# Optimization experiments

Hardware: AMD Instinct MI355X
Metric: run time of the kernel (lower is better)

Reference implementation:

```python
import jax, jax.numpy as jnp
import numpy as np

N, E, EL = 20000, 320000, 100000
IN, HID, OUT, H = 256, 128, 128, 4
NEG_SLOPE = 0.2


def setup_inputs() -> dict:
    key = jax.random.key(0)
    ks = jax.random.split(key, 20)
    g = lambda k, shape, fan: jax.random.normal(k, shape, jnp.float32) * (1.0 / np.sqrt(fan))
    inp = {
        'x': jax.random.normal(ks[0], (N, IN), jnp.float32),
        'edge_index': jax.random.randint(ks[1], (2, E), 0, N, jnp.int32),
        'edge_label_index': jax.random.randint(ks[2], (2, EL), 0, N, jnp.int32),
        # GATv2 layer 1: in -> hidden, heads=H, concat
        'W_l1': g(ks[3], (IN, H * HID), IN), 'b_l1': jnp.zeros((H * HID,), jnp.float32),
        'W_r1': g(ks[4], (IN, H * HID), IN), 'b_r1': jnp.zeros((H * HID,), jnp.float32),
        'att1': g(ks[5], (H, HID), HID), 'bias1': jnp.zeros((H * HID,), jnp.float32),
        # GATv2 layer 2: H*hidden -> out, heads=1
        'W_l2': g(ks[6], (H * HID, OUT), H * HID), 'b_l2': jnp.zeros((OUT,), jnp.float32),
        'W_r2': g(ks[7], (H * HID, OUT), H * HID), 'b_r2': jnp.zeros((OUT,), jnp.float32),
        'att2': g(ks[8], (1, OUT), OUT), 'bias2': jnp.zeros((OUT,), jnp.float32),
        # decoder: Linear(2*OUT, HID) -> GELU -> Linear(HID, 1)
        'W_d1': g(ks[9], (2 * OUT, HID), 2 * OUT), 'b_d1': jnp.zeros((HID,), jnp.float32),
        'W_d2': g(ks[10], (HID, 1), HID), 'b_d2': jnp.zeros((1,), jnp.float32),
    }
    return inp


def gatv2_conv(x, src, dst, Wl, bl, Wr, br, att, bias, heads, ch):
    n = x.shape[0]
    xl = (x @ Wl + bl).reshape(n, heads, ch)  # source transform
    xr = (x @ Wr + br).reshape(n, heads, ch)  # target transform
    xj = xl[src]                              # [E, H, C] messages from source
    xi = xr[dst]                              # [E, H, C]
    e = jax.nn.leaky_relu(xi + xj, NEG_SLOPE)
    logits = jnp.einsum('ehc,hc->eh', e, att)  # [E, H]
    # segment softmax over incoming edges of each target node
    m = jax.ops.segment_max(logits, dst, num_segments=n)
    a = jnp.exp(logits - m[dst])
    s = jax.ops.segment_sum(a, dst, num_segments=n)
    alpha = a / s[dst]
    out = jax.ops.segment_sum(alpha[..., None] * xj, dst, num_segments=n)
    return out.reshape(n, heads * ch) + bias


def reference(x, edge_index, edge_label_index,
              W_l1, b_l1, W_r1, b_r1, att1, bias1,
              W_l2, b_l2, W_r2, b_r2, att2, bias2,
              W_d1, b_d1, W_d2, b_d2):
    n = x.shape[0]
    loops = jnp.arange(n, dtype=edge_index.dtype)
    src = jnp.concatenate([edge_index[0], loops])  # add_self_loops=True (PyG default)
    dst = jnp.concatenate([edge_index[1], loops])
    z = gatv2_conv(x, src, dst, W_l1, b_l1, W_r1, b_r1, att1, bias1, H, HID)
    z = jax.nn.gelu(z)  # dropout is identity in eval mode
    z = gatv2_conv(z, src, dst, W_l2, b_l2, W_r2, b_r2, att2, bias2, 1, OUT)
    # link decoder: gather-concat-MLP
    h = jnp.concatenate([z[edge_label_index[0]], z[edge_label_index[1]]], axis=-1)
    h = jax.nn.gelu(h @ W_d1 + b_d1)
    return (h @ W_d2 + b_d2).squeeze(-1)
```

## Files before the change

kernel.cpp:

```cpp
#include <hip/hip_runtime.h>
#include <hip/hip_bf16.h>
#include <math.h>
#include <stdint.h>

using bf16 = __hip_bfloat16;
typedef unsigned short u16;
typedef unsigned int   u32;
typedef __attribute__((ext_vector_type(8))) short short8;
typedef __attribute__((ext_vector_type(4))) float f32x4;

static constexpr int NN   = 20000;
static constexpr int EE   = 320000;
static constexpr int ELN  = 100000;
static constexpr int ETOT = EE + NN;
static constexpr int INC  = 256;
static constexpr int C1   = 512;
static constexpr int C2   = 128;
static constexpr int NB   = (NN + 255) / 256;

__device__ __forceinline__ float us2f(u16 u){ union{u32 i; float f;}x; x.i=((u32)u)<<16; return x.f; }
__device__ __forceinline__ u16  f2us(float f){ union{bf16 h; u16 u;}c; c.h=__float2bfloat16(f); return c.u; }
__device__ __forceinline__ float h2f(u16 u){ union{u16 u; _Float16 h;}c; c.u=u; return (float)c.h; }
__device__ __forceinline__ float gelu_f(float x){
  float u = 1.5957691216057308f*(x + 0.044715f*x*x*x);
  float ex = __expf(u);
  float th = 1.f - 2.f/(ex + 1.f);
  return 0.5f*x*(1.f+th);
}
__device__ __forceinline__ void ld4v(const float* p, float* o){ float4 v=*(const float4*)p; o[0]=v.x;o[1]=v.y;o[2]=v.z;o[3]=v.w; }
__device__ __forceinline__ void ld4v(const u16* p, float* o){ uint2 v=*(const uint2*)p;
  o[0]=us2f(v.x&0xffff);o[1]=us2f(v.x>>16);o[2]=us2f(v.y&0xffff);o[3]=us2f(v.y>>16); }
__device__ __forceinline__ void ld4v(const _Float16* p, float* o){ uint2 v=*(const uint2*)p;
  o[0]=h2f(v.x&0xffff);o[1]=h2f(v.x>>16);o[2]=h2f(v.y&0xffff);o[3]=h2f(v.y>>16); }
__device__ __forceinline__ void ld8v(const float* p, float* o){ ld4v(p,o); ld4v(p+4,o+4); }
__device__ __forceinline__ void ld8v(const u16* p, float* o){ uint4 v=*(const uint4*)p;
  o[0]=us2f(v.x&0xffff);o[1]=us2f(v.x>>16);o[2]=us2f(v.y&0xffff);o[3]=us2f(v.y>>16);
  o[4]=us2f(v.z&0xffff);o[5]=us2f(v.z>>16);o[6]=us2f(v.w&0xffff);o[7]=us2f(v.w>>16); }
__device__ __forceinline__ void ld8v(const _Float16* p, float* o){ uint4 v=*(const uint4*)p;
  o[0]=h2f(v.x&0xffff);o[1]=h2f(v.x>>16);o[2]=h2f(v.y&0xffff);o[3]=h2f(v.y>>16);
  o[4]=h2f(v.z&0xffff);o[5]=h2f(v.z>>16);o[6]=h2f(v.w&0xffff);o[7]=h2f(v.w>>16); }
__device__ __forceinline__ void ld2v(const float* p, float* o){ float2 v=*(const float2*)p; o[0]=v.x;o[1]=v.y; }
__device__ __forceinline__ void ld2v(const _Float16* p, float* o){ u32 w=*(const u32*)p;
  o[0]=h2f(w&0xffff); o[1]=h2f(w>>16); }
__device__ __forceinline__ void st4v(float* p, const float* v){ *(float4*)p = make_float4(v[0],v[1],v[2],v[3]); }
__device__ __forceinline__ void st4v(u16* p, const float* v){ uint2 o;
  o.x=f2us(v[0])|((u32)f2us(v[1])<<16); o.y=f2us(v[2])|((u32)f2us(v[3])<<16); *(uint2*)p=o; }
__device__ __forceinline__ void st8v(float* p, const float* v){ st4v(p,v); st4v(p+4,v+4); }
__device__ __forceinline__ void st8v(u16* p, const float* v){ uint4 o;
  o.x=f2us(v[0])|((u32)f2us(v[1])<<16); o.y=f2us(v[2])|((u32)f2us(v[3])<<16);
  o.z=f2us(v[4])|((u32)f2us(v[5])<<16); o.w=f2us(v[6])|((u32)f2us(v[7])<<16); *(uint4*)p=o; }
__device__ __forceinline__ void st8v(_Float16* p, const float* v){
  union{ _Float16 h[8]; uint4 u; } c;
  #pragma unroll
  for (int j=0;j<8;++j) c.h[j] = (_Float16)v[j];
  *(uint4*)p = c.u; }

__global__ void k_hist(const int* __restrict__ ei, int* __restrict__ cnt) {
  int e = blockIdx.x*blockDim.x + threadIdx.x;
  if (e < ETOT) {
    int d = (e < EE) ? ei[EE + e] : (e - EE);
    if ((u32)d < (u32)NN) atomicAdd(&cnt[d], 1);
  }
}
__global__ void k_scan_a(const int* __restrict__ cnt, int* __restrict__ row_ptr,
                         int* __restrict__ bsum) {
  __shared__ int buf[256];
  int idx = blockIdx.x*256 + threadIdx.x;
  int v = (idx < NN) ? cnt[idx] : 0;
  buf[threadIdx.x] = v;
  __syncthreads();
  for (int off = 1; off < 256; off <<= 1) {
    int t = (threadIdx.x >= off) ? buf[threadIdx.x - off] : 0;
    __syncthreads();
    buf[threadIdx.x] += t;
    __syncthreads();
  }
  if (idx < NN) row_ptr[idx] = buf[threadIdx.x] - v;
  if (threadIdx.x == 255) bsum[blockIdx.x] = buf[255];
// ... 38 lines not shown
                                                int n) {
  for (int i = blockIdx.x*256 + threadIdx.x; i < n; i += gridDim.x*256) {
    float v = A[i];
    u16 h = f2us(v);
    Ath[i] = h;
    Atl[i] = f2us(v - us2f(h));
  }
}

struct WsArgs { const float* src[5]; u16* th[5]; u16* tl[5]; int K[5]; int N[5]; };
__global__ __launch_bounds__(256) void k_wsplit_all(WsArgs a) {
  int seg = blockIdx.y;
  int K = a.K[seg], N = a.N[seg];
  int n = K * N;
  int idx = blockIdx.x*256 + threadIdx.x;
  if (idx >= n) return;
  int nn = idx / K, k = idx - nn*K;
  float v = a.src[seg][(size_t)k*N + nn];
  u16 h = f2us(v);
  a.th[seg][idx] = h;
  a.tl[seg][idx] = f2us(v - us2f(h));
}

template <typename CT>
__global__ __launch_bounds__(256, 2)
void k_mgemm_p(const u16* __restrict__ Ath, const u16* __restrict__ Atl,
               const u16* __restrict__ Bth, const u16* __restrict__ Btl,
               const float* __restrict__ biasA, const float* __restrict__ biasB, int ncut,
               CT* __restrict__ C, int M, int N, int K) {
  __shared__ __align__(16) u16 Ah[128][32], Al[128][32];
  __shared__ __align__(16) u16 Bh[128][32], Bl[128][32];
  int tid = threadIdx.x;
  int m0 = blockIdx.x * 128, n0 = blockIdx.y * 128;
  int wave = tid >> 6, lane = tid & 63;
  int wm = (wave & 1) * 64, wn = (wave >> 1) * 64;
  int l15 = lane & 15, quad = lane >> 4;
  f32x4 acc[4][4] = {};
  int ar = tid >> 1;
  int ac = (tid & 1) * 16;
  int bn = tid >> 2;
  int bc = (tid & 3) * 8;
  uint4 z4 = make_uint4(0,0,0,0);
  for (int k0 = 0; k0 < K; k0 += 32) {
    int gr = m0 + ar;
    if (gr < M) {
      const u16* ph = &Ath[(size_t)gr*K + k0 + ac];
      const u16* pl = &Atl[(size_t)gr*K + k0 + ac];
      *(uint4*)&Ah[ar][ac]   = *(const uint4*)ph;
      *(uint4*)&Ah[ar][ac+8] = *(const uint4*)(ph+8);
      *(uint4*)&Al[ar][ac]   = *(const uint4*)pl;
      *(uint4*)&Al[ar][ac+8] = *(const uint4*)(pl+8);
    } else {
      *(uint4*)&Ah[ar][ac] = z4; *(uint4*)&Ah[ar][ac+8] = z4;
      *(uint4*)&Al[ar][ac] = z4; *(uint4*)&Al[ar][ac+8] = z4;
    }
    #pragma unroll
    for (int i = 0; i < 2; ++i) {
      int n = bn + 64*i;
      *(uint4*)&Bh[n][bc] = *(const uint4*)&Bth[(size_t)(n0+n)*K + k0 + bc];
      *(uint4*)&Bl[n][bc] = *(const uint4*)&Btl[(size_t)(n0+n)*K + k0 + bc];
    }
    __syncthreads();
    short8 af_h[4], af_l[4], bf_h[4], bf_l[4];
    #pragma unroll
    for (int i = 0; i < 4; ++i) {
      af_h[i] = *(const short8*)&Ah[wm + i*16 + l15][quad*8];
      af_l[i] = *(const short8*)&Al[wm + i*16 + l15][quad*8];
      bf_h[i] = *(const short8*)&Bh[wn + i*16 + l15][quad*8];
      bf_l[i] = *(const short8*)&Bl[wn + i*16 + l15][quad*8];
    }
    #pragma unroll
    for (int i = 0; i < 4; ++i)
      #pragma unroll
      for (int j = 0; j < 4; ++j) {
        acc[i][j] = __builtin_amdgcn_mfma_f32_16x16x32_bf16(af_h[i], bf_l[j], acc[i][j], 0,0,0);
        acc[i][j] = __builtin_amdgcn_mfma_f32_16x16x32_bf16(af_l[i], bf_h[j], acc[i][j], 0,0,0);
        acc[i][j] = __builtin_amdgcn_mfma_f32_16x16x32_bf16(af_h[i], bf_h[j], acc[i][j], 0,0,0);
      }
    __syncthreads();
  }
  #pragma unroll
  for (int j = 0; j < 4; ++j) {
    int col = n0 + wn + j*16 + l15;
    float bv = (col < ncut) ? biasA[col] : biasB[col - ncut];
    #pragma unroll
    for (int i = 0; i < 4; ++i) {
      int rbase = m0 + wm + i*16 + quad*4;
      #pragma unroll
      for (int r = 0; r < 4; ++r) {
        int row = rbase + r;
        if (row < M) C[(size_t)row*N + col] = (CT)(acc[i][j][r] + bv);
      }
    }
  }
}

template <typename AT, typename CT>
__global__ __launch_bounds__(256, 2)
void k_mgemm(const AT* __restrict__ A,
             const u16* __restrict__ Bth, const u16* __restrict__ Btl,
             const float* __restrict__ biasA, const float* __restrict__ biasB, int ncut,
             CT* __restrict__ C, int M, int N, int K) {
  __shared__ __align__(16) u16 Ah[128][32], Al[128][32];
  __shared__ __align__(16) u16 Bh[128][32], Bl[128][32];
  int tid = threadIdx.x;
  int m0 = blockIdx.x * 128, n0 = blockIdx.y * 128;
  int wave = tid >> 6, lane = tid & 63;
  int wm = (wave & 1) * 64, wn = (wave >> 1) * 64;
  int l15 = lane & 15, quad = lane >> 4;
  f32x4 acc[4][4] = {};
  int ar = tid >> 3;
  int ak = (tid & 7) * 4;
  int bn = tid >> 2;
  int bc = (tid & 3) * 8;
  for (int k0 = 0; k0 < K; k0 += 32) {
    #pragma unroll
    for (int i = 0; i < 4; ++i) {
      int row = ar + 32*i;
      int gr = m0 + row;
      float hv[4] = {0.f, 0.f, 0.f, 0.f};
      if (gr < M) ld4v(&A[(size_t)gr*K + k0 + ak], hv);
      u16 hi[4], lo[4];
      #pragma unroll
      for (int j = 0; j < 4; ++j) {
        hi[j] = f2us(hv[j]);
        lo[j] = f2us(hv[j] - us2f(hi[j]));
      }
      *(uint2*)&Ah[row][ak] = make_uint2(hi[0]|((u32)hi[1]<<16), hi[2]|((u32)hi[3]<<16));
      *(uint2*)&Al[row][ak] = make_uint2(lo[0]|((u32)lo[1]<<16), lo[2]|((u32)lo[3]<<16));
    }
    #pragma unroll
    for (int i = 0; i < 2; ++i) {
      int n = bn + 64*i;
      *(uint4*)&Bh[n][bc] = *(const uint4*)&Bth[(size_t)(n0+n)*K + k0 + bc];
      *(uint4*)&Bl[n][bc] = *(const uint4*)&Btl[(size_t)(n0+n)*K + k0 + bc];
    }
    __syncthreads();
    short8 af_h[4], af_l[4], bf_h[4], bf_l[4];
    #pragma unroll
    for (int i = 0; i < 4; ++i) {
      af_h[i] = *(const short8*)&Ah[wm + i*16 + l15][quad*8];
      af_l[i] = *(const short8*)&Al[wm + i*16 + l15][quad*8];
      bf_h[i] = *(const short8*)&Bh[wn + i*16 + l15][quad*8];
      bf_l[i] = *(const short8*)&Bl[wn + i*16 + l15][quad*8];
    }
    #pragma unroll
    for (int i = 0; i < 4; ++i)
      #pragma unroll
      for (int j = 0; j < 4; ++j) {
        acc[i][j] = __builtin_amdgcn_mfma_f32_16x16x32_bf16(af_h[i], bf_l[j], acc[i][j], 0,0,0);
        acc[i][j] = __builtin_amdgcn_mfma_f32_16x16x32_bf16(af_l[i], bf_h[j], acc[i][j], 0,0,0);
        acc[i][j] = __builtin_amdgcn_mfma_f32_16x16x32_bf16(af_h[i], bf_h[j], acc[i][j], 0,0,0);
      }
    __syncthreads();
  }
  #pragma unroll
  for (int j = 0; j < 4; ++j) {
    int col = n0 + wn + j*16 + l15;
    float bv = (col < ncut) ? biasA[col] : biasB[col - ncut];
    #pragma unroll
    for (int i = 0; i < 4; ++i) {
      int rbase = m0 + wm + i*16 + quad*4;
      #pragma unroll
      for (int r = 0; r < 4; ++r) {
        int row = rbase + r;
        if (row < M) C[(size_t)row*N + col] = (CT)(acc[i][j][r] + bv);
      }
    }
  }
}

__global__ __launch_bounds__(256, 2)
void k_dec3(const _Float16* __restrict__ z2,
            const int* __restrict__ eli,
            const u16* __restrict__ Wth, const u16* __restrict__ Wtl,
            const float* __restrict__ bd1,
            const float* __restrict__ Wd2, const float* __restrict__ bd2,
            float* __restrict__ out) {
  __shared__ __align__(16) u16 Ah[128][32], Al[128][32];
  __shared__ __align__(16) u16 Bh[128][32], Bl[128][32];
  __shared__ float pr[128][2];
  int tid = threadIdx.x;
  int e0 = blockIdx.x * 128;
  int wave = tid >> 6, lane = tid & 63;
  int wm = (wave & 1) * 64, wn = (wave >> 1) * 64;
  int l15 = lane & 15, quad = lane >> 4;
  int ar = tid >> 3;
  int ak = (tid & 7) * 4;
  int bn = tid >> 2;
  int bc = (tid & 3) * 8;
  int ia4[4], ib4[4];
  #pragma unroll
  for (int i = 0; i < 4; ++i) {
    int e = e0 + ar + 32*i;
    bool ev = e < ELN;
    int a = ev ? eli[e] : 0;      if ((u32)a >= (u32)NN) a = 0;
    int b = ev ? eli[ELN+e] : 0;  if ((u32)b >= (u32)NN) b = 0;
    ia4[i] = a; ib4[i] = b;
  }
  f32x4 acc[4][4] = {};
  for (int k0 = 0; k0 < 256; k0 += 32) {
    #pragma unroll
    for (int i = 0; i < 4; ++i) {
      int row = ar + 32*i;
      int kk = k0 + ak;
      const _Float16* src = (kk < 128) ? &z2[(size_t)ia4[i]*128 + kk]
                                       : &z2[(size_t)ib4[i]*128 + (kk - 128)];
      float hv[4];
      ld4v(src, hv);
      u16 hi[4], lo[4];
      #pragma unroll
      for (int j = 0; j < 4; ++j) {
        hi[j] = f2us(hv[j]);
        lo[j] = f2us(hv[j] - us2f(hi[j]));
      }
      *(uint2*)&Ah[row][ak] = make_uint2(hi[0]|((u32)hi[1]<<16), hi[2]|((u32)hi[3]<<16));
      *(uint2*)&Al[row][ak] = make_uint2(lo[0]|((u32)lo[1]<<16), lo[2]|((u32)lo[3]<<16));
    }
    #pragma unroll
    for (int i = 0; i < 2; ++i) {
      int n = bn + 64*i;
      *(uint4*)&Bh[n][bc] = *(const uint4*)&Wth[(size_t)n*256 + k0 + bc];
      *(uint4*)&Bl[n][bc] = *(const uint4*)&Wtl[(size_t)n*256 + k0 + bc];
    }
    __syncthreads();
    short8 af_h[4], af_l[4], bf_h[4], bf_l[4];
    #pragma unroll
    for (int i = 0; i < 4; ++i) {
      af_h[i] = *(const short8*)&Ah[wm + i*16 + l15][quad*8];
      af_l[i] = *(const short8*)&Al[wm + i*16 + l15][quad*8];
      bf_h[i] = *(const short8*)&Bh[wn + i*16 + l15][quad*8];
      bf_l[i] = *(const short8*)&Bl[wn + i*16 + l15][quad*8];
    }
    #pragma unroll
    for (int i = 0; i < 4; ++i)
      #pragma unroll
      for (int j = 0; j < 4; ++j) {
        acc[i][j] = __builtin_amdgcn_mfma_f32_16x16x32_bf16(af_h[i], bf_l[j], acc[i][j], 0,0,0);
        acc[i][j] = __builtin_amdgcn_mfma_f32_16x16x32_bf16(af_l[i], bf_h[j], acc[i][j], 0,0,0);
        acc[i][j] = __builtin_amdgcn_mfma_f32_16x16x32_bf16(af_h[i], bf_h[j], acc[i][j], 0,0,0);
      }
    __syncthreads();
  }
  float w2c[4], bbc[4];
  #pragma unroll
  for (int j = 0; j < 4; ++j) {
    int col = wn + j*16 + l15;
    w2c[j] = Wd2[col];
    bbc[j] = bd1[col];
  }
  #pragma unroll
  for (int i = 0; i < 4; ++i) {
    #pragma unroll
    for (int r = 0; r < 4; ++r) {
      float part = 0.f;
      #pragma unroll
      for (int j = 0; j < 4; ++j)
        part += gelu_f(acc[i][j][r] + bbc[j]) * w2c[j];
      part += __shfl_xor(part,1); part += __shfl_xor(part,2);
      part += __shfl_xor(part,4); part += __shfl_xor(part,8);
      if (l15 == 0) pr[wm + i*16 + quad*4 + r][wn>>6] = part;
    }
  }
  __syncthreads();
  if (tid < 128) {
    int e = e0 + tid;
    if (e < ELN) out[e] = pr[tid][0] + pr[tid][1] + bd2[0];
  }
}

template <typename AT, typename CT>
__global__ __launch_bounds__(256) void k_gemm(const AT* __restrict__ A,
                                              const float* __restrict__ W,
                                              const float* __restrict__ bias,
                                              CT* __restrict__ C,
                                              int M, int Nc, int K) {
  __shared__ __align__(16) float As[16][64];
  __shared__ __align__(16) float Bs[16][64];
  int tid = threadIdx.x;
  int m0 = blockIdx.x*64, n0 = blockIdx.y*64;
  int ty = tid >> 4, tx = tid & 15;
  int lrow = tid >> 2;
  int lk   = (tid & 3)*4;
  int wk   = tid >> 4;
  int wn   = (tid & 15)*4;
  float acc[4][4] = {};
  for (int k0 = 0; k0 < K; k0 += 16) {
    int row = m0 + lrow;
    if (row < M) {
      float a4[4]; ld4v(&A[(size_t)row*K + k0 + lk], a4);
      As[lk+0][lrow]=a4[0]; As[lk+1][lrow]=a4[1]; As[lk+2][lrow]=a4[2]; As[lk+3][lrow]=a4[3];
    } else {
      #pragma unroll
      for (int j=0;j<4;++j) As[lk+j][lrow]=0.f;
    }
    {
      float4 bv4 = *(const float4*)&W[(size_t)(k0+wk)*Nc + n0 + wn];
      Bs[wk][wn+0]=bv4.x; Bs[wk][wn+1]=bv4.y; Bs[wk][wn+2]=bv4.z; Bs[wk][wn+3]=bv4.w;
    }
    __syncthreads();
    #pragma unroll
    for (int kk=0;kk<16;++kk) {
      float4 av = *(const float4*)&As[kk][ty*4];
      float4 bv = *(const float4*)&Bs[kk][tx*4];
      float a[4]={av.x,av.y,av.z,av.w}, b[4]={bv.x,bv.y,bv.z,bv.w};
      #pragma unroll
      for (int i=0;i<4;++i)
        #pragma unroll
        for (int j=0;j<4;++j)
          acc[i][j] += a[i]*b[j];
    }
    __syncthreads();
  }
  float bv[4];
  #pragma unroll
  for (int j=0;j<4;++j) bv[j] = bias[n0 + tx*4 + j];
  #pragma unroll
  for (int i=0;i<4;++i) {
    int row = m0 + ty*4 + i;
    if (row < M) {
      float o4[4] = {acc[i][0]+bv[0], acc[i][1]+bv[1], acc[i][2]+bv[2], acc[i][3]+bv[3]};
      st4v(&C[(size_t)row*Nc + n0 + tx*4], o4);
    }
  }
}

template <typename TI, typename TO>
__global__ __launch_bounds__(256) void k_edge1(const TI* __restrict__ xl,
                                               const TI* __restrict__ xr, int ld,
                                               const float* __restrict__ att,
                                               const float* __restrict__ bias,
                                               const int* __restrict__ row_ptr,
                                               const int* __restrict__ col,
                                               TO* __restrict__ z1) {
  int wid = (blockIdx.x*blockDim.x + threadIdx.x) >> 6;
  if (wid >= NN) return;
  int lane = threadIdx.x & 63;
  int c8 = lane*8;
  float xi[8], av[8], acc[8] = {};
  ld8v(&xr[(size_t)wid*ld + c8], xi);
  #pragma unroll
  for (int j=0;j<8;++j) av[j] = att[c8+j];
  float s = 0.f;
  int e0 = row_ptr[wid], e1 = row_ptr[wid+1];
  int e = e0;
  if ((e1 - e0) & 1) {
    int sn = col[e]; if ((u32)sn >= (u32)NN) sn = 0;
    float xj[8];
    ld8v(&xl[(size_t)sn*ld + c8], xj);
    float p = 0.f;
    #pragma unroll
    for (int j=0;j<8;++j) {
      float t = xi[j] + xj[j];
      t = fmaxf(t, 0.2f*t);
      p += t*av[j];
    }
    p += __shfl_xor(p,1); p += __shfl_xor(p,2);
// ... 6 lines not shown
  }
  for (; e < e1; e += 2) {
    int s1 = col[e];   if ((u32)s1 >= (u32)NN) s1 = 0;
    int s2 = col[e+1]; if ((u32)s2 >= (u32)NN) s2 = 0;
    float xj1[8], xj2[8];
    ld8v(&xl[(size_t)s1*ld + c8], xj1);
    ld8v(&xl[(size_t)s2*ld + c8], xj2);
    float p1 = 0.f, p2 = 0.f;
    #pragma unroll
    for (int j=0;j<8;++j) {
      float t1 = xi[j] + xj1[j]; t1 = fmaxf(t1, 0.2f*t1); p1 += t1*av[j];
      float t2 = xi[j] + xj2[j]; t2 = fmaxf(t2, 0.2f*t2); p2 += t2*av[j];
    }
    p1 += __shfl_xor(p1,1); p2 += __shfl_xor(p2,1);
    p1 += __shfl_xor(p1,2); p2 += __shfl_xor(p2,2);
    p1 += __shfl_xor(p1,4); p2 += __shfl_xor(p2,4);
    p1 += __shfl_xor(p1,8); p2 += __shfl_xor(p2,8);
    float w1 = __expf(p1);
    float w2 = __expf(p2);
    s += w1 + w2;
    #pragma unroll
    for (int j=0;j<8;++j) acc[j] += w1*xj1[j] + w2*xj2[j];
  }
  float inv = 1.f/s, o[8];
  #pragma unroll
  for (int j=0;j<8;++j) o[j] = gelu_f(acc[j]*inv + bias[c8+j]);
  st8v(&z1[(size_t)wid*C1 + c8], o);
}

template <typename TI, typename TO>
__global__ __launch_bounds__(256) void k_edge2(const TI* __restrict__ xl,
                                               const TI* __restrict__ xr, int ld,
                                               const float* __restrict__ att,
                                               const float* __restrict__ bias,
                                               const int* __restrict__ row_ptr,
                                               const int* __restrict__ col,
                                               TO* __restrict__ z2) {
  int wid = (blockIdx.x*blockDim.x + threadIdx.x) >> 6;
  if (wid >= NN) return;
  int lane = threadIdx.x & 63;
  int c2 = lane*2;
  float xiv[2];
  ld2v(&xr[(size_t)wid*ld + c2], xiv);
  float a0 = att[c2], a1 = att[c2+1];
  float s = 0.f, ac0 = 0.f, ac1 = 0.f;
  int e0 = row_ptr[wid], e1 = row_ptr[wid+1];
  int e = e0;
  if ((e1 - e0) & 1) {
    int sn = col[e]; if ((u32)sn >= (u32)NN) sn = 0;
    float xj[2];
    ld2v(&xl[(size_t)sn*ld + c2], xj);
    float t0 = xiv[0] + xj[0]; t0 = fmaxf(t0, 0.2f*t0);
    float t1 = xiv[1] + xj[1]; t1 = fmaxf(t1, 0.2f*t1);
    float p = t0*a0 + t1*a1;
    p += __shfl_xor(p,1);  p += __shfl_xor(p,2);
    p += __shfl_xor(p,4);  p += __shfl_xor(p,8);
    p += __shfl_xor(p,16); p += __shfl_xor(p,32);
    float w = __expf(p);
    s += w;
    ac0 += w*xj[0];
// ... 3 lines not shown
  for (; e < e1; e += 2) {
    int s1 = col[e];   if ((u32)s1 >= (u32)NN) s1 = 0;
    int s2 = col[e+1]; if ((u32)s2 >= (u32)NN) s2 = 0;
    float xj1[2], xj2[2];
    ld2v(&xl[(size_t)s1*ld + c2], xj1);
    ld2v(&xl[(size_t)s2*ld + c2], xj2);
    float u0 = xiv[0] + xj1[0]; u0 = fmaxf(u0, 0.2f*u0);
    float u1 = xiv[1] + xj1[1]; u1 = fmaxf(u1, 0.2f*u1);
    float v0 = xiv[0] + xj2[0]; v0 = fmaxf(v0, 0.2f*v0);
    float v1 = xiv[1] + xj2[1]; v1 = fmaxf(v1, 0.2f*v1);
    float p1 = u0*a0 + u1*a1;
    float p2 = v0*a0 + v1*a1;
    p1 += __shfl_xor(p1,1);  p2 += __shfl_xor(p2,1);
    p1 += __shfl_xor(p1,2);  p2 += __shfl_xor(p2,2);
    p1 += __shfl_xor(p1,4);  p2 += __shfl_xor(p2,4);
    p1 += __shfl_xor(p1,8);  p2 += __shfl_xor(p2,8);
    p1 += __shfl_xor(p1,16); p2 += __shfl_xor(p2,16);
    p1 += __shfl_xor(p1,32); p2 += __shfl_xor(p2,32);
    float w1 = __expf(p1);
    float w2 = __expf(p2);
    s += w1 + w2;
    ac0 += w1*xj1[0] + w2*xj2[0];
    ac1 += w1*xj1[1] + w2*xj2[1];
  }
  float inv = 1.f/s;
  z2[(size_t)wid*C2 + c2]   = (TO)(ac0*inv + bias[c2]);
  z2[(size_t)wid*C2 + c2+1] = (TO)(ac1*inv + bias[c2+1]);
}

__global__ __launch_bounds__(256) void k_dec2(const float* __restrict__ z2,
                                              const int* __restrict__ eli,
                                              const float* __restrict__ Wd1,
                                              const float* __restrict__ bd1,
                                              const float* __restrict__ Wd2,
                                              const float* __restrict__ bd2,
                                              float* __restrict__ out) {
  __shared__ __align__(16) float As[16][64];
  __shared__ __align__(16) float Bs[16][128];
  int tid = threadIdx.x;
  int e0 = blockIdx.x * 64;
  int ty = tid >> 4, tx = tid & 15;
  int lrow = tid >> 2;
  int lk   = (tid & 3) * 4;
  int wk   = tid >> 4;
  int wn   = (tid & 15) * 8;
  int e = e0 + lrow;
// ... 84 lines not shown
    k_tiny<<<1, 64, 0, stream>>>(out, 16384.f + (float)mb);
    return;
  }

  size_t regA = full ? (size_t)NN*C1 : (size_t)NN*C1/2;
  char* base = (char*)d_ws;
  void* wA = base;
  void* wB = base + regA*4;
  void* wC = base + 2*regA*4;
  int* row_ptr = (int*)(base + 3*regA*4);
  int* cnt     = row_ptr + (NN + 1);
  int* col     = cnt + NN;
  int* bsum    = (int*)wA;

  hipMemsetAsync(cnt, 0, NN*sizeof(int), stream);
  k_hist<<<(ETOT+255)/256, 256, 0, stream>>>(ei, cnt);
  k_scan_a<<<NB, 256, 0, stream>>>(cnt, row_ptr, bsum);
  k_scan_b<<<1, 128, 0, stream>>>(bsum, row_ptr);
  k_scan_c<<<NB, 256, 0, stream>>>(row_ptr, bsum, cnt);
  k_scatter<<<(ETOT+255)/256, 256, 0, stream>>>(ei, cnt, col);

  if (full) {
    _Float16* xlr1 = (_Float16*)wA;
    _Float16* z1   = (_Float16*)wC;
    _Float16* xlr2 = (_Float16*)wA;
    _Float16* z2   = (_Float16*)wC;
    u16* xth = (u16*)wB;
    u16* xtl = xth + (size_t)NN*INC;
    u16* wt1th = (u16*)((char*)wB + (21u<<20));
    u16* wt1tl = wt1th + 1024*256;
    u16* wt2th = wt1tl + 1024*256;
    u16* wt2tl = wt2th + 256*512;
    u16* wdth  = wt2tl + 256*512;
    u16* wdtl  = wdth  + 128*256;

    k_xsplit<<<2048, 256, 0, stream>>>(x, xth, xtl, NN*INC);
    WsArgs wa;
    wa.src[0]=Wl1; wa.th[0]=wt1th;          wa.tl[0]=wt1tl;          wa.K[0]=INC; wa.N[0]=C1;
    wa.src[1]=Wr1; wa.th[1]=wt1th+512*256;  wa.tl[1]=wt1tl+512*256;  wa.K[1]=INC; wa.N[1]=C1;
    wa.src[2]=Wl2; wa.th[2]=wt2th;          wa.tl[2]=wt2tl;          wa.K[2]=C1;  wa.N[2]=C2;
    wa.src[3]=Wr2; wa.th[3]=wt2th+128*512;  wa.tl[3]=wt2tl+128*512;  wa.K[3]=C1;  wa.N[3]=C2;
    wa.src[4]=Wd1; wa.th[4]=wdth;           wa.tl[4]=wdtl;           wa.K[4]=256; wa.N[4]=C2;
    k_wsplit_all<<<dim3(512, 5), 256, 0, stream>>>(wa);

    dim3 gm1((NN+127)/128, 1024/128);
    k_mgemm_p<_Float16><<<gm1, 256, 0, stream>>>(xth, xtl, wt1th, wt1tl,
                                                 bl1, br1, 512, xlr1, NN, 1024, INC);
    k_edge1<_Float16,_Float16><<<NN/4, 256, 0, stream>>>(xlr1, xlr1+512, 1024,
                                                         att1, bias1, row_ptr, col, z1);
    dim3 gm2((NN+127)/128, 256/128);
    k_mgemm<_Float16,_Float16><<<gm2, 256, 0, stream>>>(z1, wt2th, wt2tl,
                                                        bl2, br2, 128, xlr2, NN, 256, C1);
    k_edge2<_Float16,_Float16><<<NN/4, 256, 0, stream>>>(xlr2, xlr2+128, 256,
                                                         att2, bias2, row_ptr, col, z2);
    k_dec3<<<(ELN+127)/128, 256, 0, stream>>>(z2, eli, wdth, wdtl, bd1, Wd2, bd2, out);
  } else {
    u16* xl1 = (u16*)wA;
    u16* xr1 = (u16*)wB;
    u16* z1  = (u16*)wC;
    float* xl2 = (float*)wA;
    float* xr2 = (float*)wB;
    float* z2  = (float*)wC;
    dim3 g1((NN+63)/64, C1/64);
    dim3 g2((NN+63)/64, C2/64);
    k_gemm<float,u16><<<g1, 256, 0, stream>>>(x, Wl1, bl1, xl1, NN, C1, INC);
    k_gemm<float,u16><<<g1, 256, 0, stream>>>(x, Wr1, br1, xr1, NN, C1, INC);
    k_edge1<u16,u16><<<NN/4, 256, 0, stream>>>(xl1, xr1, C1, att1, bias1, row_ptr, col, z1);
    k_gemm<u16,float><<<g2, 256, 0, stream>>>(z1, Wl2, bl2, xl2, NN, C2, C1);
    k_gemm<u16,float><<<g2, 256, 0, stream>>>(z1, Wr2, br2, xr2, NN, C2, C1);
    k_edge2<float,float><<<NN/4, 256, 0, stream>>>(xl2, xr2, C2, att2, bias2, row_ptr, col, z2);
    k_dec2<<<(ELN+63)/64, 256, 0, stream>>>(z2, eli, Wd1, bd1, Wd2, bd2, out);
  }
}
```

Baseline: 392.2 us.

## Load GEMM tiles directly to LDS and emit pre-split bf16 activations from edge kernels

The MFMA GEMMs now stage A/B tiles with global_load_lds (direct global-to-LDS copies), one wave per operand, instead of register round-trips. The edge kernels write outputs pre-split into bf16 hi/lo pairs, so the layer-2 GEMM and decoder no longer split activations on the fly. The GEMM epilogue goes through LDS for coalesced 128-bit stores, and block indexing is remapped so N-tiles of the same M-rows run adjacently. The costs are double the bytes for the z1/z2 intermediates and a serial load-sync-compute loop with no double buffering.

Result: no change. 389.0 us (-0.8%).

```diff
diff --git a/kernel.cpp b/kernel.cpp
--- a/kernel.cpp
+++ b/kernel.cpp
@@ -27,11 +27,13 @@
   float th = 1.f - 2.f/(ex + 1.f);
   return 0.5f*x*(1.f+th);
 }
+__device__ __forceinline__ void gl_lds16(const u16* g, void* l) {
+  __builtin_amdgcn_global_load_lds((const __attribute__((address_space(1))) void*)g,
+                                   (__attribute__((address_space(3))) void*)l, 16, 0, 0);
+}
 __device__ __forceinline__ void ld4v(const float* p, float* o){ float4 v=*(const float4*)p; o[0]=v.x;o[1]=v.y;o[2]=v.z;o[3]=v.w; }
 __device__ __forceinline__ void ld4v(const u16* p, float* o){ uint2 v=*(const uint2*)p;
   o[0]=us2f(v.x&0xffff);o[1]=us2f(v.x>>16);o[2]=us2f(v.y&0xffff);o[3]=us2f(v.y>>16); }
-__device__ __forceinline__ void ld4v(const _Float16* p, float* o){ uint2 v=*(const uint2*)p;
-  o[0]=h2f(v.x&0xffff);o[1]=h2f(v.x>>16);o[2]=h2f(v.y&0xffff);o[3]=h2f(v.y>>16); }
 __device__ __forceinline__ void ld8v(const float* p, float* o){ ld4v(p,o); ld4v(p+4,o+4); }
 __device__ __forceinline__ void ld8v(const u16* p, float* o){ uint4 v=*(const uint4*)p;
   o[0]=us2f(v.x&0xffff);o[1]=us2f(v.x>>16);o[2]=us2f(v.y&0xffff);o[3]=us2f(v.y>>16);
@@ -49,11 +51,6 @@
 __device__ __forceinline__ void st8v(u16* p, const float* v){ uint4 o;
   o.x=f2us(v[0])|((u32)f2us(v[1])<<16); o.y=f2us(v[2])|((u32)f2us(v[3])<<16);
   o.z=f2us(v[4])|((u32)f2us(v[5])<<16); o.w=f2us(v[6])|((u32)f2us(v[7])<<16); *(uint4*)p=o; }
-__device__ __forceinline__ void st8v(_Float16* p, const float* v){
-  union{ _Float16 h[8]; uint4 u; } c;
-  #pragma unroll
-  for (int j=0;j<8;++j) c.h[j] = (_Float16)v[j];
-  *(uint4*)p = c.u; }
 
 __global__ void k_hist(const int* __restrict__ ei, int* __restrict__ cnt) {
   int e = blockIdx.x*blockDim.x + threadIdx.x;
@@ -138,52 +135,39 @@
   a.tl[seg][idx] = f2us(v - us2f(h));
 }
 
-template <typename CT>
 __global__ __launch_bounds__(256, 2)
-void k_mgemm_p(const u16* __restrict__ Ath, const u16* __restrict__ Atl,
+void k_mgemm_a(const u16* __restrict__ Ath, const u16* __restrict__ Atl,
                const u16* __restrict__ Bth, const u16* __restrict__ Btl,
                const float* __restrict__ biasA, const float* __restrict__ biasB, int ncut,
-               CT* __restrict__ C, int M, int N, int K) {
-  __shared__ __align__(16) u16 Ah[128][32], Al[128][32];
-  __shared__ __align__(16) u16 Bh[128][32], Bl[128][32];
+               _Float16* __restrict__ C, int M, int N, int K, int nby) {
+  __shared__ __align__(16) u16 sm[17408];
   int tid = threadIdx.x;
-  int m0 = blockIdx.x * 128, n0 = blockIdx.y * 128;
+  int bidy = blockIdx.x % nby, bidx = blockIdx.x / nby;
+  int m0 = bidx * 128, n0 = bidy * 128;
   int wave = tid >> 6, lane = tid & 63;
   int wm = (wave & 1) * 64, wn = (wave >> 1) * 64;
   int l15 = lane & 15, quad = lane >> 4;
+  const u16* pbase = (wave == 0) ? Ath : (wave == 1) ? Atl : (wave == 2) ? Bth : Btl;
+  bool isA = wave < 2;
+  int rbase = isA ? m0 : n0;
+  int rseg = lane >> 2;
+  int kseg = (lane & 3) * 8;
   f32x4 acc[4][4] = {};
-  int ar = tid >> 1;
-  int ac = (tid & 1) * 16;
-  int bn = tid >> 2;
-  int bc = (tid & 3) * 8;
-  uint4 z4 = make_uint4(0,0,0,0);
   for (int k0 = 0; k0 < K; k0 += 32) {
-    int gr = m0 + ar;
-    if (gr < M) {
-      const u16* ph = &Ath[(size_t)gr*K + k0 + ac];
-      const u16* pl = &Atl[(size_t)gr*K + k0 + ac];
-      *(uint4*)&Ah[ar][ac]   = *(const uint4*)ph;
-      *(uint4*)&Ah[ar][ac+8] = *(const uint4*)(ph+8);
-      *(uint4*)&Al[ar][ac]   = *(const uint4*)pl;
-      *(uint4*)&Al[ar][ac+8] = *(const uint4*)(pl+8);
-    } else {
-      *(uint4*)&Ah[ar][ac] = z4; *(uint4*)&Ah[ar][ac+8] = z4;
-      *(uint4*)&Al[ar][ac] = z4; *(uint4*)&Al[ar][ac+8] = z4;
-    }
-    #pragma unroll
-    for (int i = 0; i < 2; ++i) {
-      int n = bn + 64*i;
-      *(uint4*)&Bh[n][bc] = *(const uint4*)&Bth[(size_t)(n0+n)*K + k0 + bc];
-      *(uint4*)&Bl[n][bc] = *(const uint4*)&Btl[(size_t)(n0+n)*K + k0 + bc];
+    #pragma unroll
+    for (int i = 0; i < 8; ++i) {
+      int r = rbase + i*16 + rseg;
+      if (isA && r > M-1) r = M-1;
+      gl_lds16(&pbase[(size_t)r*K + k0 + kseg], (char*)sm + (wave<<13) + (i<<10));
     }
     __syncthreads();
     short8 af_h[4], af_l[4], bf_h[4], bf_l[4];
     #pragma unroll
     for (int i = 0; i < 4; ++i) {
-      af_h[i] = *(const short8*)&Ah[wm + i*16 + l15][quad*8];
-      af_l[i] = *(const short8*)&Al[wm + i*16 + l15][quad*8];
-      bf_h[i] = *(const short8*)&Bh[wn + i*16 + l15][quad*8];
-      bf_l[i] = *(const short8*)&Bl[wn + i*16 + l15][quad*8];
+      af_h[i] = *(const short8*)&sm[         (wm + i*16 + l15)*32 + quad*8];
+      af_l[i] = *(const short8*)&sm[ 4096 +  (wm + i*16 + l15)*32 + quad*8];
+      bf_h[i] = *(const short8*)&sm[ 8192 +  (wn + i*16 + l15)*32 + quad*8];
+      bf_l[i] = *(const short8*)&sm[12288 +  (wn + i*16 + l15)*32 + quad*8];
     }
     #pragma unroll
     for (int i = 0; i < 4; ++i)
@@ -197,156 +181,81 @@
   }
   #pragma unroll
   for (int j = 0; j < 4; ++j) {
-    int col = n0 + wn + j*16 + l15;
-    float bv = (col < ncut) ? biasA[col] : biasB[col - ncut];
+    int col = wn + j*16 + l15;
+    int colg = n0 + col;
+    float bv = (colg < ncut) ? biasA[colg] : biasB[colg - ncut];
     #pragma unroll
     for (int i = 0; i < 4; ++i) {
-      int rbase = m0 + wm + i*16 + quad*4;
+      int rowb = wm + i*16 + quad*4;
       #pragma unroll
       for (int r = 0; r < 4; ++r) {
-        int row = rbase + r;
-        if (row < M) C[(size_t)row*N + col] = (CT)(acc[i][j][r] + bv);
+        union { _Float16 h; u16 u; } cv;
+        cv.h = (_Float16)(acc[i][j][r] + bv);
+        sm[(rowb + r)*136 + col] = cv.u;
       }
     }
   }
-}
-
-template <typename AT, typename CT>
+  __syncthreads();
+  int row = tid >> 1, half = (tid & 1) * 64;
+  int gr = m0 + row;
+  if (gr < M) {
+    uint4* d = (uint4*)&C[(size_t)gr*N + n0 + half];
+    const uint4* s = (const uint4*)&sm[row*136 + half];
+    #pragma unroll
+    for (int q = 0; q < 8; ++q) d[q] = s[q];
+  }
+}
+
 __global__ __launch_bounds__(256, 2)
-void k_mgemm(const AT* __restrict__ A,
-             const u16* __restrict__ Bth, const u16* __restrict__ Btl,
-             const float* __restrict__ biasA, const float* __restrict__ biasB, int ncut,
-             CT* __restrict__ C, int M, int N, int K) {
-  __shared__ __align__(16) u16 Ah[128][32], Al[128][32];
-  __shared__ __align__(16) u16 Bh[128][32], Bl[128][32];
-  int tid = threadIdx.x;
-  int m0 = blockIdx.x * 128, n0 = blockIdx.y * 128;
-  int wave = tid >> 6, lane = tid & 63;
-  int wm = (wave & 1) * 64, wn = (wave >> 1) * 64;
-  int l15 = lane & 15, quad = lane >> 4;
-  f32x4 acc[4][4] = {};
-  int ar = tid >> 3;
-  int ak = (tid & 7) * 4;
-  int bn = tid >> 2;
-  int bc = (tid & 3) * 8;
-  for (int k0 = 0; k0 < K; k0 += 32) {
-    #pragma unroll
-    for (int i = 0; i < 4; ++i) {
-      int row = ar + 32*i;
-      int gr = m0 + row;
-      float hv[4] = {0.f, 0.f, 0.f, 0.f};
-      if (gr < M) ld4v(&A[(size_t)gr*K + k0 + ak], hv);
-      u16 hi[4], lo[4];
-      #pragma unroll
-      for (int j = 0; j < 4; ++j) {
-        hi[j] = f2us(hv[j]);
-        lo[j] = f2us(hv[j] - us2f(hi[j]));
-      }
-      *(uint2*)&Ah[row][ak] = make_uint2(hi[0]|((u32)hi[1]<<16), hi[2]|((u32)hi[3]<<16));
-      *(uint2*)&Al[row][ak] = make_uint2(lo[0]|((u32)lo[1]<<16), lo[2]|((u32)lo[3]<<16));
-    }
-    #pragma unroll
-    for (int i = 0; i < 2; ++i) {
-      int n = bn + 64*i;
-      *(uint4*)&Bh[n][bc] = *(const uint4*)&Bth[(size_t)(n0+n)*K + k0 + bc];
-      *(uint4*)&Bl[n][bc] = *(const uint4*)&Btl[(size_t)(n0+n)*K + k0 + bc];
-    }
-    __syncthreads();
-    short8 af_h[4], af_l[4], bf_h[4], bf_l[4];
-    #pragma unroll
-    for (int i = 0; i < 4; ++i) {
-      af_h[i] = *(const short8*)&Ah[wm + i*16 + l15][quad*8];
-      af_l[i] = *(const short8*)&Al[wm + i*16 + l15][quad*8];
-      bf_h[i] = *(const short8*)&Bh[wn + i*16 + l15][quad*8];
-      bf_l[i] = *(const short8*)&Bl[wn + i*16 + l15][quad*8];
-    }
-    #pragma unroll
-    for (int i = 0; i < 4; ++i)
-      #pragma unroll
-      for (int j = 0; j < 4; ++j) {
-        acc[i][j] = __builtin_amdgcn_mfma_f32_16x16x32_bf16(af_h[i], bf_l[j], acc[i][j], 0,0,0);
-        acc[i][j] = __builtin_amdgcn_mfma_f32_16x16x32_bf16(af_l[i], bf_h[j], acc[i][j], 0,0,0);
-        acc[i][j] = __builtin_amdgcn_mfma_f32_16x16x32_bf16(af_h[i], bf_h[j], acc[i][j], 0,0,0);
-      }
-    __syncthreads();
-  }
-  #pragma unroll
-  for (int j = 0; j < 4; ++j) {
-    int col = n0 + wn + j*16 + l15;
-    float bv = (col < ncut) ? biasA[col] : biasB[col - ncut];
-    #pragma unroll
-    for (int i = 0; i < 4; ++i) {
-      int rbase = m0 + wm + i*16 + quad*4;
-      #pragma unroll
-      for (int r = 0; r < 4; ++r) {
-        int row = rbase + r;
-        if (row < M) C[(size_t)row*N + col] = (CT)(acc[i][j][r] + bv);
-      }
-    }
-  }
-}
-
-__global__ __launch_bounds__(256, 2)
-void k_dec3(const _Float16* __restrict__ z2,
+void k_dec4(const u16* __restrict__ z2h, const u16* __restrict__ z2l,
             const int* __restrict__ eli,
             const u16* __restrict__ Wth, const u16* __restrict__ Wtl,
             const float* __restrict__ bd1,
             const float* __restrict__ Wd2, const float* __restrict__ bd2,
             float* __restrict__ out) {
-  __shared__ __align__(16) u16 Ah[128][32], Al[128][32];
-  __shared__ __align__(16) u16 Bh[128][32], Bl[128][32];
+  __shared__ __align__(16) u16 sm[16384];
   __shared__ float pr[128][2];
+  __shared__ int ias[128], ibs[128];
   int tid = threadIdx.x;
   int e0 = blockIdx.x * 128;
+  if (tid < 128) {
+    int e = e0 + tid;
+    bool ev = e < ELN;
+    int a = ev ? eli[e] : 0;      if ((u32)a >= (u32)NN) a = 0;
+    int b = ev ? eli[ELN+e] : 0;  if ((u32)b >= (u32)NN) b = 0;
+    ias[tid] = a; ibs[tid] = b;
+  }
+  __syncthreads();
   int wave = tid >> 6, lane = tid & 63;
   int wm = (wave & 1) * 64, wn = (wave >> 1) * 64;
   int l15 = lane & 15, quad = lane >> 4;
-  int ar = tid >> 3;
-  int ak = (tid & 7) * 4;
-  int bn = tid >> 2;
-  int bc = (tid & 3) * 8;
-  int ia4[4], ib4[4];
-  #pragma unroll
-  for (int i = 0; i < 4; ++i) {
-    int e = e0 + ar + 32*i;
-    bool ev = e < ELN;
-    int a = ev ? eli[e] : 0;      if ((u32)a >= (u32)NN) a = 0;
-    int b = ev ? eli[ELN+e] : 0;  if ((u32)b >= (u32)NN) b = 0;
-    ia4[i] = a; ib4[i] = b;
-  }
+  const u16* pbase = (wave == 0) ? z2h : (wave == 1) ? z2l : (wave == 2) ? Wth : Wtl;
+  bool isA = wave < 2;
+  int rseg = lane >> 2;
+  int kseg = (lane & 3) * 8;
   f32x4 acc[4][4] = {};
   for (int k0 = 0; k0 < 256; k0 += 32) {
     #pragma unroll
+    for (int i = 0; i < 8; ++i) {
+      int r = i*16 + rseg;
+      const u16* g;
+      if (isA) {
+        int node = (k0 < 128) ? ias[r] : ibs[r];
+        int kk   = (k0 < 128) ? k0 : (k0 - 128);
+        g = &pbase[(size_t)node*128 + kk + kseg];
+      } else {
+        g = &pbase[(size_t)r*256 + k0 + kseg];
+      }
+      gl_lds16(g, (char*)sm + (wave<<13) + (i<<10));
+    }
+    __syncthreads();
+    short8 af_h[4], af_l[4], bf_h[4], bf_l[4];
+    #pragma unroll
     for (int i = 0; i < 4; ++i) {
-      int row = ar + 32*i;
-      int kk = k0 + ak;
-      const _Float16* src = (kk < 128) ? &z2[(size_t)ia4[i]*128 + kk]
-                                       : &z2[(size_t)ib4[i]*128 + (kk - 128)];
-      float hv[4];
-      ld4v(src, hv);
-      u16 hi[4], lo[4];
-      #pragma unroll
-      for (int j = 0; j < 4; ++j) {
-        hi[j] = f2us(hv[j]);
-        lo[j] = f2us(hv[j] - us2f(hi[j]));
-      }
-      *(uint2*)&Ah[row][ak] = make_uint2(hi[0]|((u32)hi[1]<<16), hi[2]|((u32)hi[3]<<16));
-      *(uint2*)&Al[row][ak] = make_uint2(lo[0]|((u32)lo[1]<<16), lo[2]|((u32)lo[3]<<16));
-    }
-    #pragma unroll
-    for (int i = 0; i < 2; ++i) {
-      int n = bn + 64*i;
-      *(uint4*)&Bh[n][bc] = *(const uint4*)&Wth[(size_t)n*256 + k0 + bc];
-      *(uint4*)&Bl[n][bc] = *(const uint4*)&Wtl[(size_t)n*256 + k0 + bc];
-    }
-    __syncthreads();
-    short8 af_h[4], af_l[4], bf_h[4], bf_l[4];
-    #pragma unroll
-    for (int i = 0; i < 4; ++i) {
-      af_h[i] = *(const short8*)&Ah[wm + i*16 + l15][quad*8];
-      af_l[i] = *(const short8*)&Al[wm + i*16 + l15][quad*8];
-      bf_h[i] = *(const short8*)&Bh[wn + i*16 + l15][quad*8];
-      bf_l[i] = *(const short8*)&Bl[wn + i*16 + l15][quad*8];
+      af_h[i] = *(const short8*)&sm[         (wm + i*16 + l15)*32 + quad*8];
+      af_l[i] = *(const short8*)&sm[ 4096 +  (wm + i*16 + l15)*32 + quad*8];
+      bf_h[i] = *(const short8*)&sm[ 8192 +  (wn + i*16 + l15)*32 + quad*8];
+      bf_l[i] = *(const short8*)&sm[12288 +  (wn + i*16 + l15)*32 + quad*8];
     }
     #pragma unroll
     for (int i = 0; i < 4; ++i)
@@ -385,70 +294,13 @@
   }
 }
 
-template <typename AT, typename CT>
-__global__ __launch_bounds__(256) void k_gemm(const AT* __restrict__ A,
-                                              const float* __restrict__ W,
-                                              const float* __restrict__ bias,
-                                              CT* __restrict__ C,
-                                              int M, int Nc, int K) {
-  __shared__ __align__(16) float As[16][64];
-  __shared__ __align__(16) float Bs[16][64];
-  int tid = threadIdx.x;
-  int m0 = blockIdx.x*64, n0 = blockIdx.y*64;
-  int ty = tid >> 4, tx = tid & 15;
-  int lrow = tid >> 2;
-  int lk   = (tid & 3)*4;
-  int wk   = tid >> 4;
-  int wn   = (tid & 15)*4;
-  float acc[4][4] = {};
-  for (int k0 = 0; k0 < K; k0 += 16) {
-    int row = m0 + lrow;
-    if (row < M) {
-      float a4[4]; ld4v(&A[(size_t)row*K + k0 + lk], a4);
-      As[lk+0][lrow]=a4[0]; As[lk+1][lrow]=a4[1]; As[lk+2][lrow]=a4[2]; As[lk+3][lrow]=a4[3];
-    } else {
-      #pragma unroll
-      for (int j=0;j<4;++j) As[lk+j][lrow]=0.f;
-    }
-    {
-      float4 bv4 = *(const float4*)&W[(size_t)(k0+wk)*Nc + n0 + wn];
-      Bs[wk][wn+0]=bv4.x; Bs[wk][wn+1]=bv4.y; Bs[wk][wn+2]=bv4.z; Bs[wk][wn+3]=bv4.w;
-    }
-    __syncthreads();
-    #pragma unroll
-    for (int kk=0;kk<16;++kk) {
-      float4 av = *(const float4*)&As[kk][ty*4];
-      float4 bv = *(const float4*)&Bs[kk][tx*4];
-      float a[4]={av.x,av.y,av.z,av.w}, b[4]={bv.x,bv.y,bv.z,bv.w};
-      #pragma unroll
-      for (int i=0;i<4;++i)
-        #pragma unroll
-        for (int j=0;j<4;++j)
-          acc[i][j] += a[i]*b[j];
-    }
-    __syncthreads();
-  }
-  float bv[4];
-  #pragma unroll
-  for (int j=0;j<4;++j) bv[j] = bias[n0 + tx*4 + j];
-  #pragma unroll
-  for (int i=0;i<4;++i) {
-    int row = m0 + ty*4 + i;
-    if (row < M) {
-      float o4[4] = {acc[i][0]+bv[0], acc[i][1]+bv[1], acc[i][2]+bv[2], acc[i][3]+bv[3]};
-      st4v(&C[(size_t)row*Nc + n0 + tx*4], o4);
-    }
-  }
-}
-
-template <typename TI, typename TO>
-__global__ __launch_bounds__(256) void k_edge1(const TI* __restrict__ xl,
-                                               const TI* __restrict__ xr, int ld,
-                                               const float* __restrict__ att,
-                                               const float* __restrict__ bias,
-                                               const int* __restrict__ row_ptr,
-                                               const int* __restrict__ col,
-                                               TO* __restrict__ z1) {
+__global__ __launch_bounds__(256) void k_edge1p(const _Float16* __restrict__ xl,
+                                                const _Float16* __restrict__ xr, int ld,
+                                                const float* __restrict__ att,
+                                                const float* __restrict__ bias,
+                                                const int* __restrict__ row_ptr,
+                                                const int* __restrict__ col,
+                                                u16* __restrict__ z1h, u16* __restrict__ z1l) {
   int wid = (blockIdx.x*blockDim.x + threadIdx.x) >> 6;
   if (wid >= NN) return;
   int lane = threadIdx.x & 63;
@@ -501,20 +353,30 @@
     #pragma unroll
     for (int j=0;j<8;++j) acc[j] += w1*xj1[j] + w2*xj2[j];
   }
-  float inv = 1.f/s, o[8];
-  #pragma unroll
-  for (int j=0;j<8;++j) o[j] = gelu_f(acc[j]*inv + bias[c8+j]);
-  st8v(&z1[(size_t)wid*C1 + c8], o);
-}
-
-template <typename TI, typename TO>
-__global__ __launch_bounds__(256) void k_edge2(const TI* __restrict__ xl,
-                                               const TI* __restrict__ xr, int ld,
-                                               const float* __restrict__ att,
-                                               const float* __restrict__ bias,
-                                               const int* __restrict__ row_ptr,
-                                               const int* __restrict__ col,
-                                               TO* __restrict__ z2) {
+  float inv = 1.f/s;
+  u16 hh[8], ll[8];
+  #pragma unroll
+  for (int j=0;j<8;++j) {
+    float o = gelu_f(acc[j]*inv + bias[c8+j]);
+    hh[j] = f2us(o);
+    ll[j] = f2us(o - us2f(hh[j]));
+  }
+  uint4 H, L;
+  H.x = hh[0]|((u32)hh[1]<<16); H.y = hh[2]|((u32)hh[3]<<16);
+  H.z = hh[4]|((u32)hh[5]<<16); H.w = hh[6]|((u32)hh[7]<<16);
+  L.x = ll[0]|((u32)ll[1]<<16); L.y = ll[2]|((u32)ll[3]<<16);
+  L.z = ll[4]|((u32)ll[5]<<16); L.w = ll[6]|((u32)ll[7]<<16);
+  *(uint4*)&z1h[(size_t)wid*C1 + c8] = H;
+  *(uint4*)&z1l[(size_t)wid*C1 + c8] = L;
+}
+
+__global__ __launch_bounds__(256) void k_edge2p(const _Float16* __restrict__ xl,
+                                                const _Float16* __restrict__ xr, int ld,
+                                                const float* __restrict__ att,
+                                                const float* __restrict__ bias,
+                                                const int* __restrict__ row_ptr,
+                                                const int* __restrict__ col,
+                                                u16* __restrict__ z2h, u16* __restrict__ z2l) {
   int wid = (blockIdx.x*blockDim.x + threadIdx.x) >> 6;
   if (wid >= NN) return;
   int lane = threadIdx.x & 63;
@@ -564,6 +426,145 @@
     s += w1 + w2;
     ac0 += w1*xj1[0] + w2*xj2[0];
     ac1 += w1*xj1[1] + w2*xj2[1];
+  }
+  float inv = 1.f/s;
+  float o0 = ac0*inv + bias[c2];
+  float o1 = ac1*inv + bias[c2+1];
+  u16 h0 = f2us(o0), h1 = f2us(o1);
+  u16 l0 = f2us(o0 - us2f(h0)), l1v = f2us(o1 - us2f(h1));
+  *(u32*)&z2h[(size_t)wid*C2 + c2] = h0 | ((u32)h1 << 16);
+  *(u32*)&z2l[(size_t)wid*C2 + c2] = l0 | ((u32)l1v << 16);
+}
+
+template <typename AT, typename CT>
+__global__ __launch_bounds__(256) void k_gemm(const AT* __restrict__ A,
+                                              const float* __restrict__ W,
+                                              const float* __restrict__ bias,
+                                              CT* __restrict__ C,
+                                              int M, int Nc, int K) {
+  __shared__ __align__(16) float As[16][64];
+  __shared__ __align__(16) float Bs[16][64];
+  int tid = threadIdx.x;
+  int m0 = blockIdx.x*64, n0 = blockIdx.y*64;
+  int ty = tid >> 4, tx = tid & 15;
+  int lrow = tid >> 2;
+  int lk   = (tid & 3)*4;
+  int wk   = tid >> 4;
+  int wn   = (tid & 15)*4;
+  float acc[4][4] = {};
+  for (int k0 = 0; k0 < K; k0 += 16) {
+    int row = m0 + lrow;
+    if (row < M) {
+      float a4[4]; ld4v(&A[(size_t)row*K + k0 + lk], a4);
+      As[lk+0][lrow]=a4[0]; As[lk+1][lrow]=a4[1]; As[lk+2][lrow]=a4[2]; As[lk+3][lrow]=a4[3];
+    } else {
+      #pragma unroll
+      for (int j=0;j<4;++j) As[lk+j][lrow]=0.f;
+    }
+    {
+      float4 bv4 = *(const float4*)&W[(size_t)(k0+wk)*Nc + n0 + wn];
+      Bs[wk][wn+0]=bv4.x; Bs[wk][wn+1]=bv4.y; Bs[wk][wn+2]=bv4.z; Bs[wk][wn+3]=bv4.w;
+    }
+    __syncthreads();
+    #pragma unroll
+    for (int kk=0;kk<16;++kk) {
+      float4 av = *(const float4*)&As[kk][ty*4];
+      float4 bv = *(const float4*)&Bs[kk][tx*4];
+      float a[4]={av.x,av.y,av.z,av.w}, b[4]={bv.x,bv.y,bv.z,bv.w};
+      #pragma unroll
+      for (int i=0;i<4;++i)
+        #pragma unroll
+        for (int j=0;j<4;++j)
+          acc[i][j] += a[i]*b[j];
+    }
+    __syncthreads();
+  }
+  float bv[4];
+  #pragma unroll
+  for (int j=0;j<4;++j) bv[j] = bias[n0 + tx*4 + j];
+  #pragma unroll
+  for (int i=0;i<4;++i) {
+    int row = m0 + ty*4 + i;
+    if (row < M) {
+      float o4[4] = {acc[i][0]+bv[0], acc[i][1]+bv[1], acc[i][2]+bv[2], acc[i][3]+bv[3]};
+      st4v(&C[(size_t)row*Nc + n0 + tx*4], o4);
+    }
+  }
+}
+
+template <typename TI, typename TO>
+__global__ __launch_bounds__(256) void k_edge1c(const TI* __restrict__ xl,
+                                                const TI* __restrict__ xr, int ld,
+                                                const float* __restrict__ att,
+                                                const float* __restrict__ bias,
+                                                const int* __restrict__ row_ptr,
+                                                const int* __restrict__ col,
+                                                TO* __restrict__ z1) {
+  int wid = (blockIdx.x*blockDim.x + threadIdx.x) >> 6;
+  if (wid >= NN) return;
+  int lane = threadIdx.x & 63;
+  int c8 = lane*8;
+  float xi[8], av[8], acc[8] = {};
+  ld8v(&xr[(size_t)wid*ld + c8], xi);
+  #pragma unroll
+  for (int j=0;j<8;++j) av[j] = att[c8+j];
+  float s = 0.f;
+  int e0 = row_ptr[wid], e1 = row_ptr[wid+1];
+  for (int e = e0; e < e1; ++e) {
+    int sn = col[e]; if ((u32)sn >= (u32)NN) sn = 0;
+    float xj[8];
+    ld8v(&xl[(size_t)sn*ld + c8], xj);
+    float p = 0.f;
+    #pragma unroll
+    for (int j=0;j<8;++j) {
+      float t = xi[j] + xj[j];
+      t = fmaxf(t, 0.2f*t);
+      p += t*av[j];
+    }
+    p += __shfl_xor(p,1); p += __shfl_xor(p,2);
+    p += __shfl_xor(p,4); p += __shfl_xor(p,8);
+    float w = __expf(p);
+    s += w;
+    #pragma unroll
+    for (int j=0;j<8;++j) acc[j] += w*xj[j];
+  }
+  float inv = 1.f/s, o[8];
+  #pragma unroll
+  for (int j=0;j<8;++j) o[j] = gelu_f(acc[j]*inv + bias[c8+j]);
+  st8v(&z1[(size_t)wid*C1 + c8], o);
+}
+
+template <typename TI, typename TO>
+__global__ __launch_bounds__(256) void k_edge2c(const TI* __restrict__ xl,
+                                                const TI* __restrict__ xr, int ld,
+                                                const float* __restrict__ att,
+                                                const float* __restrict__ bias,
+                                                const int* __restrict__ row_ptr,
+                                                const int* __restrict__ col,
+                                                TO* __restrict__ z2) {
+  int wid = (blockIdx.x*blockDim.x + threadIdx.x) >> 6;
+  if (wid >= NN) return;
+  int lane = threadIdx.x & 63;
+  int c2 = lane*2;
+  float xiv[2];
+  ld2v(&xr[(size_t)wid*ld + c2], xiv);
+  float a0 = att[c2], a1 = att[c2+1];
+  float s = 0.f, ac0 = 0.f, ac1 = 0.f;
+  int e0 = row_ptr[wid], e1 = row_ptr[wid+1];
+  for (int e = e0; e < e1; ++e) {
+    int sn = col[e]; if ((u32)sn >= (u32)NN) sn = 0;
+    float xj[2];
+    ld2v(&xl[(size_t)sn*ld + c2], xj);
+    float t0 = xiv[0] + xj[0]; t0 = fmaxf(t0, 0.2f*t0);
+    float t1 = xiv[1] + xj[1]; t1 = fmaxf(t1, 0.2f*t1);
+    float p = t0*a0 + t1*a1;
+    p += __shfl_xor(p,1);  p += __shfl_xor(p,2);
+    p += __shfl_xor(p,4);  p += __shfl_xor(p,8);
+    p += __shfl_xor(p,16); p += __shfl_xor(p,32);
+    float w = __expf(p);
+    s += w;
+    ac0 += w*xj[0];
+    ac1 += w*xj[1];
   }
   float inv = 1.f/s;
   z2[(size_t)wid*C2 + c2]   = (TO)(ac0*inv + bias[c2]);
@@ -694,9 +695,7 @@
 
   if (full) {
     _Float16* xlr1 = (_Float16*)wA;
-    _Float16* z1   = (_Float16*)wC;
     _Float16* xlr2 = (_Float16*)wA;
-    _Float16* z2   = (_Float16*)wC;
     u16* xth = (u16*)wB;
     u16* xtl = xth + (size_t)NN*INC;
     u16* wt1th = (u16*)((char*)wB + (21u<<20));
@@ -705,6 +704,10 @@
     u16* wt2tl = wt2th + 256*512;
     u16* wdth  = wt2tl + 256*512;
     u16* wdtl  = wdth  + 128*256;
+    u16* z1h = (u16*)wC;
+    u16* z1l = z1h + (size_t)NN*C1;
+    u16* z2h = (u16*)wC;
+    u16* z2l = z2h + (size_t)NN*C2;
 
     k_xsplit<<<2048, 256, 0, stream>>>(x, xth, xtl, NN*INC);
     WsArgs wa;
@@ -715,17 +718,13 @@
     wa.src[4]=Wd1; wa.th[4]=wdth;           wa.tl[4]=wdtl;           wa.K[4]=256; wa.N[4]=C2;
     k_wsplit_all<<<dim3(512, 5), 256, 0, stream>>>(wa);
 
-    dim3 gm1((NN+127)/128, 1024/128);
-    k_mgemm_p<_Float16><<<gm1, 256, 0, stream>>>(xth, xtl, wt1th, wt1tl,
-                                                 bl1, br1, 512, xlr1, NN, 1024, INC);
-    k_edge1<_Float16,_Float16><<<NN/4, 256, 0, stream>>>(xlr1, xlr1+512, 1024,
-                                                         att1, bias1, row_ptr, col, z1);
-    dim3 gm2((NN+127)/128, 256/128);
-    k_mgemm<_Float16,_Float16><<<gm2, 256, 0, stream>>>(z1, wt2th, wt2tl,
-                                                        bl2, br2, 128, xlr2, NN, 256, C1);
-    k_edge2<_Float16,_Float16><<<NN/4, 256, 0, stream>>>(xlr2, xlr2+128, 256,
-                                                         att2, bias2, row_ptr, col, z2);
-    k_dec3<<<(ELN+127)/128, 256, 0, stream>>>(z2, eli, wdth, wdtl, bd1, Wd2, bd2, out);
+    k_mgemm_a<<<157*8, 256, 0, stream>>>(xth, xtl, wt1th, wt1tl,
+                                         bl1, br1, 512, xlr1, NN, 1024, INC, 8);
+    k_edge1p<<<NN/4, 256, 0, stream>>>(xlr1, xlr1+512, 1024, att1, bias1, row_ptr, col, z1h, z1l);
+    k_mgemm_a<<<157*2, 256, 0, stream>>>(z1h, z1l, wt2th, wt2tl,
+                                         bl2, br2, 128, xlr2, NN, 256, C1, 2);
+    k_edge2p<<<NN/4, 256, 0, stream>>>(xlr2, xlr2+128, 256, att2, bias2, row_ptr, col, z2h, z2l);
+    k_dec4<<<(ELN+127)/128, 256, 0, stream>>>(z2h, z2l, eli, wdth, wdtl, bd1, Wd2, bd2, out);
   } else {
     u16* xl1 = (u16*)wA;
     u16* xr1 = (u16*)wB;
@@ -737,10 +736,10 @@
     dim3 g2((NN+63)/64, C2/64);
     k_gemm<float,u16><<<g1, 256, 0, stream>>>(x, Wl1, bl1, xl1, NN, C1, INC);
     k_gemm<float,u16><<<g1, 256, 0, stream>>>(x, Wr1, br1, xr1, NN, C1, INC);
-    k_edge1<u16,u16><<<NN/4, 256, 0, stream>>>(xl1, xr1, C1, att1, bias1, row_ptr, col, z1);
+    k_edge1c<u16,u16><<<NN/4, 256, 0, stream>>>(xl1, xr1, C1, att1, bias1, row_ptr, col, z1);
     k_gemm<u16,float><<<g2, 256, 0, stream>>>(z1, Wl2, bl2, xl2, NN, C2, C1);
     k_gemm<u16,float><<<g2, 256, 0, stream>>>(z1, Wr2, br2, xr2, NN, C2, C1);
-    k_edge2<float,float><<<NN/4, 256, 0, stream>>>(xl2, xr2, C2, att2, bias2, row_ptr, col, z2);
+    k_edge2c<float,float><<<NN/4, 256, 0, stream>>>(xl2, xr2, C2, att2, bias2, row_ptr, col, z2);
     k_dec2<<<(ELN+63)/64, 256, 0, stream>>>(z2, eli, Wd1, bd1, Wd2, bd2, out);
   }
 }
```
